# Kernel tuning notes

Measured on AMD Instinct MI355X. Metric: run time of the kernel, lower is better.

Reference implementation:

```python
import jax, jax.numpy as jnp
import numpy as np

N = 100000
E = 800000
D_IN = 64
D_OUT = 64
SCALES = (4, 8)


def setup_inputs() -> dict:
    key = jax.random.key(0)
    ks = jax.random.split(key, 8)
    x = jax.random.normal(ks[0], (N, D_IN), dtype=jnp.float32)
    edge_index = jax.random.randint(ks[1], (2, E), 0, N, dtype=jnp.int64)
    s = 1.0 / np.sqrt(D_IN)
    W1 = jax.random.uniform(ks[2], (D_OUT, D_IN), minval=-s, maxval=s, dtype=jnp.float32)
    b1 = jax.random.uniform(ks[3], (D_OUT,), minval=-s, maxval=s, dtype=jnp.float32)
    W2 = jax.random.uniform(ks[4], (D_OUT, D_IN), minval=-s, maxval=s, dtype=jnp.float32)
    b2 = jax.random.uniform(ks[5], (D_OUT,), minval=-s, maxval=s, dtype=jnp.float32)
    sg = 1.0 / np.sqrt(D_OUT * len(SCALES))
    Wg = jax.random.uniform(ks[6], (D_OUT, D_OUT * len(SCALES)), minval=-sg, maxval=sg, dtype=jnp.float32)
    bg = jax.random.uniform(ks[7], (D_OUT,), minval=-sg, maxval=sg, dtype=jnp.float32)
    return {"x": x, "edge_index": edge_index, "W1": W1, "b1": b1,
            "W2": W2, "b2": b2, "Wg": Wg, "bg": bg}


def _gconv(x, src, tgt, W, b):
    # scatter-add neighbor features: agg[src] += x[tgt]
    agg = jax.ops.segment_sum(x[tgt], src, num_segments=N)  # [N, D_IN]
    counts = jax.ops.segment_sum(jnp.ones((src.shape[0], 1), x.dtype), src,
                                 num_segments=N) + 1e-6     # [N, 1]
    agg = agg / counts
    return agg @ W.T + b                                    # [N, D_OUT]


def reference(x, edge_index, W1, b1, W2, b2, Wg, bg):
    k_max = E // N  # = 8
    outs = []
    for scale, (W, b) in zip(SCALES, ((W1, b1), (W2, b2))):
        scale = min(scale, k_max)
        src = edge_index[0, :N * scale]
        tgt = edge_index[1, :N * scale]
        outs.append(_gconv(x, src, tgt, W, b))
    multi = jnp.concatenate(outs, axis=-1)                   # [N, 2*D_OUT]
    gate = jax.nn.sigmoid(multi @ Wg.T + bg)                 # [N, D_OUT]
    fused = gate * outs[0] + (1.0 - gate) * outs[1]
    return fused
```

## Files before the change

### kernel.cpp

```cpp
#include <hip/hip_runtime.h>
#include <hip/hip_bf16.h>

#define N_NODES 100000
#define E_TOTAL 800000
#define E1      400000
#define D       64
#define CAP     32

#define NPB        256
#define NB         ((N_NODES + NPB - 1) / NPB)
#define BSTRIDE    (NPB * CAP)
#define BCAP       3072
#define EPB        4096
#define NBKT_BLKS  ((E_TOTAL + EPB - 1) / EPB)
#define PREP_TPB   512
#define EPT        (EPB / PREP_TPB)
#define NBP        512

typedef short s16x8 __attribute__((ext_vector_type(8)));
typedef float f32x4 __attribute__((ext_vector_type(4)));
typedef unsigned u32x4 __attribute__((ext_vector_type(4)));

#define WS_CNT     0
#define WS_ENTRIES (N_NODES)
#define WS_W1B     (WS_ENTRIES + N_NODES * CAP)
#define WS_W2B     (WS_W1B + 2048)
#define WS_WGB     (WS_W2B + 2048)
#define WS_BIAS    (WS_WGB + 4096)
#define WS_CUR     (WS_BIAS + 192)
#define WS_XB      (WS_CUR + 512)
#define WS_NEED_BYTES ((size_t)(WS_XB + (size_t)N_NODES * D / 2) * 4)

#define XCONV_BLOCKS ((N_NODES * D / 16 + PREP_TPB - 1) / PREP_TPB)
#define WCONV_BLOCKS 5

__device__ __forceinline__ float ldv(const void* p, size_t idx, int fp32)
{
    return fp32 ? ((const float*)p)[idx]
                : __bfloat162float(((const __hip_bfloat16*)p)[idx]);
}

__device__ __forceinline__ void detect2(const int* ei, const unsigned short* xu,
                                        int* s2, int& e64, int& fp32)
{
    if (threadIdx.x == 0) { s2[0] = 0; s2[1] = 0; }
    __syncthreads();
    if (threadIdx.x < 16 && ei[2 * threadIdx.x + 1] != 0) atomicOr(&s2[0], 1);
    { unsigned u = xu[threadIdx.x]; if (((u >> 7) & 0xFF) >= 0x90) atomicOr(&s2[1], 1); }
    __syncthreads();
    e64 = (s2[0] == 0); fp32 = s2[1];
}

__global__ __launch_bounds__(512) void prep_kernel(
    const void* __restrict__ xv, const int* __restrict__ ei,
    const void* __restrict__ W1v, const void* __restrict__ b1v,
    const void* __restrict__ W2v, const void* __restrict__ b2v,
    const void* __restrict__ Wgv, const void* __restrict__ bgv,
    unsigned* __restrict__ ws, int use_xb)
{
    __shared__ int s2[2];
    __shared__ unsigned hist[NB];
    __shared__ unsigned sc[NBP];
    __shared__ unsigned gbase[NB];
    __shared__ unsigned sorted_s[EPB];
    __shared__ unsigned short bkt_s[EPB];
    int e64, fp32;
    detect2(ei, (const unsigned short*)xv, s2, e64, fp32);

    const int tid = threadIdx.x;

    if (blockIdx.x < NBKT_BLKS) {
        for (int j = tid; j < NB; j += PREP_TPB) hist[j] = 0;
        __syncthreads();

        const int e0 = blockIdx.x * EPB;
        int srcv[EPT], tgtv[EPT];
        if (e64) {
#pragma unroll
            for (int i = 0; i < EPT; ++i) {
                const int e  = e0 + i * PREP_TPB + tid;
                const int ec = min(e, E_TOTAL - 1);
                srcv[i] = (int)((const uint2*)ei)[ec].x;
                tgtv[i] = (int)((const uint2*)ei)[E_TOTAL + ec].x;
                if (e >= E_TOTAL) srcv[i] = -1;
            }
        } else {
#pragma unroll
            for (int i = 0; i < EPT; ++i) {
                const int e  = e0 + i * PREP_TPB + tid;
                const int ec = min(e, E_TOTAL - 1);
                srcv[i] = ei[ec];
                tgtv[i] = ei[E_TOTAL + ec];
                if (e >= E_TOTAL) srcv[i] = -1;
            }
        }

        unsigned recv[EPT], br[EPT];
#pragma unroll
        for (int i = 0; i < EPT; ++i) {
            const int e = e0 + i * PREP_TPB + tid;
            br[i] = 0xFFFFFFFFu;
            if (srcv[i] >= 0) {
                const unsigned b = (unsigned)srcv[i] >> 8;
                const unsigned r = atomicAdd(&hist[b], 1u);
                recv[i] = (unsigned)tgtv[i]
                        | ((e < E1) ? 0x20000u : 0u)
                        | (((unsigned)srcv[i] & (NPB - 1)) << 18);
                br[i] = (b << 16) | r;
            }
        }
        __syncthreads();

        sc[tid] = (tid < NB) ? hist[tid] : 0u;
        __syncthreads();
        for (int s = 1; s < NBP; s <<= 1) {
            const unsigned v = (tid >= s) ? sc[tid - s] : 0u;
            __syncthreads();
            sc[tid] += v;
            __syncthreads();
        }

        for (int j = tid; j < NB; j += PREP_TPB) {
            const unsigned h = hist[j];
            gbase[j] = h ? atomicAdd(ws + WS_CUR + j, h) : 0u;
        }
        __syncthreads();

#pragma unroll
        for (int i = 0; i < EPT; ++i) {
            if (br[i] != 0xFFFFFFFFu) {
                const unsigned b = br[i] >> 16, r = br[i] & 0xFFFFu;
                const unsigned pos = (sc[b] - hist[b]) + r;
                sorted_s[pos] = recv[i];
                bkt_s[pos] = (unsigned short)b;
            }
        }
        __syncthreads();

        const unsigned tot = sc[NB - 1];
        for (unsigned k = tid; k < tot; k += PREP_TPB) {
            const unsigned b = bkt_s[k];
            const unsigned g = gbase[b] + (k - (sc[b] - hist[b]));
            if (g < BCAP)
                ws[WS_ENTRIES + (size_t)b * BSTRIDE + g] = sorted_s[k];
        }
        return;
    }

    const int bx = (int)blockIdx.x - NBKT_BLKS;
    if (bx < XCONV_BLOCKS) {
        if (use_xb && fp32) {
            const int gid = bx * PREP_TPB + tid;
            if (gid < N_NODES * D / 16) {
                __hip_bfloat16* Xb = (__hip_bfloat16*)(ws + WS_XB);
                const f32x4* src4 = (const f32x4*)xv + (size_t)gid * 4;
#pragma unroll
                for (int h = 0; h < 2; ++h) {
                    const f32x4 v0 = src4[2 * h];
                    const f32x4 v1 = src4[2 * h + 1];
                    s16x8 o;
#pragma unroll
                    for (int j = 0; j < 4; ++j) {
                        o[j]     = (short)__bfloat16_as_ushort(__float2bfloat16(v0[j]));
                        o[4 + j] = (short)__bfloat16_as_ushort(__float2bfloat16(v1[j]));
                    }
                    *(s16x8*)(Xb + (size_t)gid * 16 + h * 8) = o;
                }
            }
        }
        return;
    }

    const int gid = (bx - XCONV_BLOCKS) * PREP_TPB + tid;
    __hip_bfloat16* W1b = (__hip_bfloat16*)(ws + WS_W1B);
    __hip_bfloat16* W2b = (__hip_bfloat16*)(ws + WS_W2B);
    __hip_bfloat16* Wgb = (__hip_bfloat16*)(ws + WS_WGB);
    float* bias = (float*)(ws + WS_BIAS);

    if (gid < 2048) {
#pragma unroll
        for (int k = 0; k < 8; ++k) {
            const int i = gid * 8 + k;
            if (i < 4096)       W1b[i]        = __float2bfloat16(ldv(W1v, i, fp32));
            else if (i < 8192)  W2b[i - 4096] = __float2bfloat16(ldv(W2v, i - 4096, fp32));
            else                Wgb[i - 8192] = __float2bfloat16(ldv(Wgv, i - 8192, fp32));
        }
    } else if (gid < 2072) {
        const int j = gid - 2048;
#pragma unroll
        for (int k = 0; k < 8; ++k) {
            const int i = j * 8 + k;
            if (i < 64)       bias[i] = ldv(b1v, i, fp32);
            else if (i < 128) bias[i] = ldv(b2v, i - 64, fp32);
            else              bias[i] = ldv(bgv, i - 128, fp32);
        }
    }
}

__global__ __launch_bounds__(256) void csr_kernel(unsigned* __restrict__ ws)
{
    __shared__ unsigned rec_s[BCAP];
    __shared__ __align__(16) unsigned ent[NPB * CAP];
    __shared__ unsigned n1c[NPB], ctc[NPB], a1[NPB], a2[NPB];

    const int b  = blockIdx.x;
    const int n0 = b * NPB;
    const int nn = min(NPB, N_NODES - n0);

    for (int j = threadIdx.x; j < NPB; j += 256) { n1c[j] = 0; ctc[j] = 0; }
    {
        const u32x4 z = {0u, 0u, 0u, 0u};
        for (int j = threadIdx.x; j < NPB * CAP / 4; j += 256) ((u32x4*)ent)[j] = z;
    }
    const unsigned C = min(ws[WS_CUR + b], (unsigned)BCAP);
    for (unsigned r = threadIdx.x; r < C; r += 256)
        rec_s[r] = ws[WS_ENTRIES + (size_t)b * BSTRIDE + r];
    __syncthreads();

    for (unsigned r = threadIdx.x; r < C; r += 256) {
        const unsigned rec = rec_s[r];
        const unsigned sl  = rec >> 18;
        atomicAdd(&ctc[sl], 1u);
        if (rec & 0x20000u) atomicAdd(&n1c[sl], 1u);
    }
    __syncthreads();
    for (int j = threadIdx.x; j < NPB; j += 256) {
        a1[j] = 0u;
        a2[j] = min(n1c[j], (unsigned)CAP);
    }
    __syncthreads();
    for (unsigned r = threadIdx.x; r < C; r += 256) {
        const unsigned rec = rec_s[r];
        const unsigned sl  = rec >> 18;
        unsigned p;
        if (rec & 0x20000u) p = atomicAdd(&a1[sl], 1u);
        else                p = atomicAdd(&a2[sl], 1u);
        if (p < CAP) ent[sl * CAP + p] = rec & 0x1FFFFu;
    }
    __syncthreads();

    const int tot4 = (nn * CAP) / 4;
    u32x4* dst = (u32x4*)(ws + WS_ENTRIES + (size_t)n0 * CAP);
    const u32x4* srcp = (const u32x4*)ent;
    for (int j = threadIdx.x; j < tot4; j += 256) dst[j] = srcp[j];

    if (threadIdx.x < nn) {
        const unsigned ct = min(ctc[threadIdx.x], 0xFFFFu);
        const unsigned p1 = min(n1c[threadIdx.x], (unsigned)CAP);
        ws[WS_CNT + n0 + threadIdx.x] = ct | (p1 << 16);
    }
}

__global__ __launch_bounds__(256) void fused_kernel(
    const unsigned* __restrict__ ws, const void* __restrict__ xv,
    void* __restrict__ outv, int use_xb)
{
    __shared__ __align__(16) __hip_bfloat16 sS[16][136];
    __shared__ __align__(16) __hip_bfloat16 sO[16][136];
    __shared__ int s2d[2];

    if (threadIdx.x == 0) s2d[0] = 0;
    __syncthreads();
    { unsigned u = ((const unsigned short*)xv)[threadIdx.x];
      if (((u >> 7) & 0xFF) >= 0x90) atomicOr(&s2d[0], 1); }
    __syncthreads();
    const int fp32 = s2d[0];

    const int w    = threadIdx.x >> 6;
    const int lane = threadIdx.x & 63;
    const int base = blockIdx.x * 16;

    unsigned entv[4], cw[4];
#pragma unroll
    for (int i = 0; i < 4; ++i) {
        const int n = base + w * 4 + i;
        cw[i]   = ws[WS_CNT + n];
        entv[i] = ws[WS_ENTRIES + (size_t)n * CAP + (lane & 31)];
    }
    int degc[4], p1c[4]; unsigned degt[4];
#pragma unroll
    for (int i = 0; i < 4; ++i) {
        degt[i] = cw[i] & 0xFFFFu;
        p1c[i]  = (int)(cw[i] >> 16);
        degc[i] = (int)min(degt[i], (unsigned)CAP);
    }

    const int half = lane >> 5;
    const int cc   = lane & 31;

    float s1x[4], s1y[4], s2x[4], s2y[4];
#pragma unroll
    for (int i = 0; i < 4; ++i) { s1x[i] = s1y[i] = s2x[i] = s2y[i] = 0.f; }

    int rmax = 0;
#pragma unroll
    for (int i = 0; i < 4; ++i) rmax = max(rmax, (degc[i] + 1) >> 1);
    rmax = (rmax + 1) & ~1;

    const int direct_f32 = (fp32 && !use_xb);
    if (!direct_f32) {
        const char* xb = fp32 ? (const char*)(ws + WS_XB) : (const char*)xv;
        const unsigned ccb = (unsigned)cc << 2;
#pragma unroll 2
        for (int r = 0; r < rmax; ++r) {
#pragma unroll
            for (int i = 0; i < 4; ++i) {
                const int j = 2 * r + half;
                const unsigned en = (unsigned)__shfl((int)entv[i], j);
                unsigned u = *(const unsigned*)(xb + (size_t)((en << 7) + ccb));
                u = (j < degc[i]) ? u : 0u;
                const float fx = __uint_as_float(u << 16);
                const float fy = __uint_as_float(u & 0xFFFF0000u);
                const float fl = (j < p1c[i]) ? 1.f : 0.f;
                s2x[i] += fx; s2y[i] += fy;
                s1x[i] = fmaf(fl, fx, s1x[i]); s1y[i] = fmaf(fl, fy, s1y[i]);
            }
        }
    } else {
        const char* xb = (const char*)xv;
        const unsigned ccb = (unsigned)cc << 3;
#pragma unroll 2
        for (int r = 0; r < rmax; ++r) {
#pragma unroll
            for (int i = 0; i < 4; ++i) {
                const int j = 2 * r + half;
                const unsigned en = (unsigned)__shfl((int)entv[i], j);
                const uint2 u = *(const uint2*)(xb + (size_t)((en << 8) + ccb));
                const bool val = j < degc[i];
                const float fx = val ? __uint_as_float(u.x) : 0.f;
                const float fy = val ? __uint_as_float(u.y) : 0.f;
                const float fl = (j < p1c[i]) ? 1.f : 0.f;
                s2x[i] += fx; s2y[i] += fy;
                s1x[i] = fmaf(fl, fx, s1x[i]); s1y[i] = fmaf(fl, fy, s1y[i]);
            }
        }
    }

#pragma unroll
    for (int i = 0; i < 4; ++i) {
        const int nl = w * 4 + i;
        float a = s1x[i], b = s1y[i], c = s2x[i], d = s2y[i];
        a += __shfl_xor(a, 32); b += __shfl_xor(b, 32);
        c += __shfl_xor(c, 32); d += __shfl_xor(d, 32);
        const float inv1 = 1.0f / ((float)p1c[i] + 1e-6f);
        const float inv2 = 1.0f / ((float)degt[i] + 1e-6f);
        if (lane < 32) {
            const __hip_bfloat162 p1 = __float22bfloat162_rn({a * inv1, b * inv1});
            const __hip_bfloat162 p2 = __float22bfloat162_rn({c * inv2, d * inv2});
            *(__hip_bfloat162*)&sS[nl][2 * cc]      = p1;
            *(__hip_bfloat162*)&sS[nl][64 + 2 * cc] = p2;
        }
    }
    __syncthreads();

    const int m = lane & 15;
    const int q = lane >> 4;
    const int nd = w * 16 + m;

    const s16x8* W1b = (const s16x8*)(ws + WS_W1B);
    const s16x8* W2b = (const s16x8*)(ws + WS_W2B);
    const s16x8* Wgb = (const s16x8*)(ws + WS_WGB);
    const float* bias = (const float*)(ws + WS_BIAS);

    const s16x8 a1c0 = *(const s16x8*)&sS[m][q * 8];
    const s16x8 a1c1 = *(const s16x8*)&sS[m][32 + q * 8];
    const s16x8 a2c0 = *(const s16x8*)&sS[m][64 + q * 8];
    const s16x8 a2c1 = *(const s16x8*)&sS[m][96 + q * 8];

    f32x4 z = {0.f, 0.f, 0.f, 0.f};
    z = __builtin_amdgcn_mfma_f32_16x16x32_bf16(a1c0, W1b[nd * 8 + q],     z, 0, 0, 0);
    z = __builtin_amdgcn_mfma_f32_16x16x32_bf16(a1c1, W1b[nd * 8 + 4 + q], z, 0, 0, 0);
    f32x4 y = {0.f, 0.f, 0.f, 0.f};
    y = __builtin_amdgcn_mfma_f32_16x16x32_bf16(a2c0, W2b[nd * 8 + q],     y, 0, 0, 0);
    y = __builtin_amdgcn_mfma_f32_16x16x32_bf16(a2c1, W2b[nd * 8 + 4 + q], y, 0, 0, 0);
    const float bb1 = bias[nd], bb2 = bias[64 + nd];
#pragma unroll
    for (int r = 0; r < 4; ++r) { z[r] += bb1; y[r] += bb2; }

#pragma unroll
    for (int r = 0; r < 4; ++r) {
        sO[q * 4 + r][nd]      = __float2bfloat16(z[r]);
        sO[q * 4 + r][64 + nd] = __float2bfloat16(y[r]);
    }
    __syncthreads();

    s16x8 ga[4];
#pragma unroll
    for (int c = 0; c < 4; ++c)
        ga[c] = *(const s16x8*)&sO[m][c * 32 + q * 8];

    f32x4 g4 = {0.f, 0.f, 0.f, 0.f};
#pragma unroll
    for (int c = 0; c < 4; ++c)
        g4 = __builtin_amdgcn_mfma_f32_16x16x32_bf16(ga[c], Wgb[nd * 16 + c * 4 + q], g4, 0, 0, 0);
    const float bbg = bias[128 + nd];

#pragma unroll
    for (int r = 0; r < 4; ++r) {
        const float g = 1.0f / (1.0f + __expf(-(g4[r] + bbg)));
        const float v = g * z[r] + (1.0f - g) * y[r];
        const size_t node = (size_t)(base + q * 4 + r);
        if (fp32) ((float*)outv)[node * 64 + nd] = v;
        else      ((__hip_bfloat16*)outv)[node * 64 + nd] = __float2bfloat16(v);
    }
}

extern "C" void kernel_launch(void* const* d_in, const int* in_sizes, int n_in,
                              void* d_out, int out_size, void* d_ws, size_t ws_size,
                              hipStream_t stream)
{
    const void* x  = d_in[0];
    const int*  ei = (const int*)d_in[1];
    unsigned* ws = (unsigned*)d_ws;

    const int use_xb = (ws_size >= WS_NEED_BYTES) ? 1 : 0;

    hipMemsetAsync(ws + WS_CUR, 0, NB * sizeof(unsigned), stream);
    prep_kernel<<<NBKT_BLKS + XCONV_BLOCKS + WCONV_BLOCKS, PREP_TPB, 0, stream>>>(
        x, ei, d_in[2], d_in[3], d_in[4], d_in[5], d_in[6], d_in[7], ws, use_xb);
    csr_kernel<<<NB, 256, 0, stream>>>(ws);
    fused_kernel<<<N_NODES / 16, 256, 0, stream>>>(ws, x, d_out, use_xb);
}
```

Measured before the change: 151.4 us.

## Merge prep and CSR kernels into one cooperative kernel with grid sync

Folds the bucket-sort prep kernel and the per-bucket CSR build kernel into a single cooperative launch of 512 blocks, separated by a grid-wide barrier, which removes one kernel launch and its drain/fill gap. The sort phase now uses 2048 edges per block and a wave-shuffle scan instead of a barrier-heavy shared-memory scan, and the x bf16 conversion runs as a grid-strided loop over fewer blocks. In exchange it relies on all 512 blocks being co-resident with 48KB of shared memory each. The CSR phase now uses 512 threads, so half the threads idle in per-node loops.

```diff
diff --git a/kernel.cpp b/kernel.cpp
--- a/kernel.cpp
+++ b/kernel.cpp
@@ -1,5 +1,8 @@
 #include <hip/hip_runtime.h>
 #include <hip/hip_bf16.h>
+#include <hip/hip_cooperative_groups.h>
+
+namespace cg = cooperative_groups;
 
 #define N_NODES 100000
 #define E_TOTAL 800000
@@ -11,11 +14,12 @@
 #define NB         ((N_NODES + NPB - 1) / NPB)
 #define BSTRIDE    (NPB * CAP)
 #define BCAP       3072
-#define EPB        4096
-#define NBKT_BLKS  ((E_TOTAL + EPB - 1) / EPB)
-#define PREP_TPB   512
-#define EPT        (EPB / PREP_TPB)
-#define NBP        512
+#define EPB        2048
+#define NSORT      ((E_TOTAL + EPB - 1) / EPB)
+#define K1_TPB     512
+#define EPT        (EPB / K1_TPB)
+#define XCONV_B    120
+#define GRID1      512
 
 typedef short s16x8 __attribute__((ext_vector_type(8)));
 typedef float f32x4 __attribute__((ext_vector_type(4)));
@@ -31,9 +35,6 @@
 #define WS_XB      (WS_CUR + 512)
 #define WS_NEED_BYTES ((size_t)(WS_XB + (size_t)N_NODES * D / 2) * 4)
 
-#define XCONV_BLOCKS ((N_NODES * D / 16 + PREP_TPB - 1) / PREP_TPB)
-#define WCONV_BLOCKS 5
-
 __device__ __forceinline__ float ldv(const void* p, size_t idx, int fp32)
 {
     return fp32 ? ((const float*)p)[idx]
@@ -51,7 +52,7 @@
     e64 = (s2[0] == 0); fp32 = s2[1];
 }
 
-__global__ __launch_bounds__(512) void prep_kernel(
+__global__ __launch_bounds__(512) void build_kernel(
     const void* __restrict__ xv, const int* __restrict__ ei,
     const void* __restrict__ W1v, const void* __restrict__ b1v,
     const void* __restrict__ W2v, const void* __restrict__ b2v,
@@ -59,26 +60,33 @@
     unsigned* __restrict__ ws, int use_xb)
 {
     __shared__ int s2[2];
-    __shared__ unsigned hist[NB];
-    __shared__ unsigned sc[NBP];
-    __shared__ unsigned gbase[NB];
-    __shared__ unsigned sorted_s[EPB];
-    __shared__ unsigned short bkt_s[EPB];
+    __shared__ unsigned wsum[8], wpre[8];
+    __shared__ __align__(16) unsigned lraw[12288];
+
     int e64, fp32;
     detect2(ei, (const unsigned short*)xv, s2, e64, fp32);
 
-    const int tid = threadIdx.x;
-
-    if (blockIdx.x < NBKT_BLKS) {
-        for (int j = tid; j < NB; j += PREP_TPB) hist[j] = 0;
-        __syncthreads();
-
-        const int e0 = blockIdx.x * EPB;
+    const int tid  = threadIdx.x;
+    const int bid  = blockIdx.x;
+    const int lane = tid & 63;
+    const int wid  = tid >> 6;
+
+    if (bid < NSORT) {
+        unsigned* hist   = lraw;
+        unsigned* sc     = lraw + 512;
+        unsigned* gbase  = lraw + 1024;
+        unsigned* sorted = lraw + 1536;
+        unsigned short* bkt = (unsigned short*)(lraw + 1536 + 2048);
+
+        for (int j = tid; j < NB; j += K1_TPB) hist[j] = 0;
+        __syncthreads();
+
+        const int e0 = bid * EPB;
         int srcv[EPT], tgtv[EPT];
         if (e64) {
 #pragma unroll
             for (int i = 0; i < EPT; ++i) {
-                const int e  = e0 + i * PREP_TPB + tid;
+                const int e  = e0 + i * K1_TPB + tid;
                 const int ec = min(e, E_TOTAL - 1);
                 srcv[i] = (int)((const uint2*)ei)[ec].x;
                 tgtv[i] = (int)((const uint2*)ei)[E_TOTAL + ec].x;
@@ -87,7 +95,7 @@
         } else {
 #pragma unroll
             for (int i = 0; i < EPT; ++i) {
-                const int e  = e0 + i * PREP_TPB + tid;
+                const int e  = e0 + i * K1_TPB + tid;
                 const int ec = min(e, E_TOTAL - 1);
                 srcv[i] = ei[ec];
                 tgtv[i] = ei[E_TOTAL + ec];
@@ -98,7 +106,7 @@
         unsigned recv[EPT], br[EPT];
 #pragma unroll
         for (int i = 0; i < EPT; ++i) {
-            const int e = e0 + i * PREP_TPB + tid;
+            const int e = e0 + i * K1_TPB + tid;
             br[i] = 0xFFFFFFFFu;
             if (srcv[i] >= 0) {
                 const unsigned b = (unsigned)srcv[i] >> 8;
@@ -111,16 +119,24 @@
         }
         __syncthreads();
 
-        sc[tid] = (tid < NB) ? hist[tid] : 0u;
-        __syncthreads();
-        for (int s = 1; s < NBP; s <<= 1) {
-            const unsigned v = (tid >= s) ? sc[tid - s] : 0u;
-            __syncthreads();
-            sc[tid] += v;
-            __syncthreads();
-        }
-
-        for (int j = tid; j < NB; j += PREP_TPB) {
+        unsigned v = (tid < NB) ? hist[tid] : 0u;
+#pragma unroll
+        for (int s = 1; s < 64; s <<= 1) {
+            const unsigned t = __shfl_up(v, s);
+            if (lane >= s) v += t;
+        }
+        if (lane == 63) wsum[wid] = v;
+        __syncthreads();
+        if (tid == 0) {
+            unsigned acc = 0;
+#pragma unroll
+            for (int k = 0; k < 8; ++k) { acc += wsum[k]; wpre[k] = acc; }
+        }
+        __syncthreads();
+        if (wid) v += wpre[wid - 1];
+        if (tid < NB) sc[tid] = v;
+
+        for (int j = tid; j < NB; j += K1_TPB) {
             const unsigned h = hist[j];
             gbase[j] = h ? atomicAdd(ws + WS_CUR + j, h) : 0u;
         }
@@ -131,123 +147,118 @@
             if (br[i] != 0xFFFFFFFFu) {
                 const unsigned b = br[i] >> 16, r = br[i] & 0xFFFFu;
                 const unsigned pos = (sc[b] - hist[b]) + r;
-                sorted_s[pos] = recv[i];
-                bkt_s[pos] = (unsigned short)b;
+                sorted[pos] = recv[i];
+                bkt[pos] = (unsigned short)b;
             }
         }
         __syncthreads();
 
         const unsigned tot = sc[NB - 1];
-        for (unsigned k = tid; k < tot; k += PREP_TPB) {
-            const unsigned b = bkt_s[k];
+        for (unsigned k = tid; k < tot; k += K1_TPB) {
+            const unsigned b = bkt[k];
             const unsigned g = gbase[b] + (k - (sc[b] - hist[b]));
             if (g < BCAP)
-                ws[WS_ENTRIES + (size_t)b * BSTRIDE + g] = sorted_s[k];
-        }
-        return;
-    }
-
-    const int bx = (int)blockIdx.x - NBKT_BLKS;
-    if (bx < XCONV_BLOCKS) {
+                ws[WS_ENTRIES + (size_t)b * BSTRIDE + g] = sorted[k];
+        }
+    } else if (bid < NSORT + XCONV_B) {
         if (use_xb && fp32) {
-            const int gid = bx * PREP_TPB + tid;
-            if (gid < N_NODES * D / 16) {
-                __hip_bfloat16* Xb = (__hip_bfloat16*)(ws + WS_XB);
-                const f32x4* src4 = (const f32x4*)xv + (size_t)gid * 4;
-#pragma unroll
-                for (int h = 0; h < 2; ++h) {
-                    const f32x4 v0 = src4[2 * h];
-                    const f32x4 v1 = src4[2 * h + 1];
-                    s16x8 o;
-#pragma unroll
-                    for (int j = 0; j < 4; ++j) {
-                        o[j]     = (short)__bfloat16_as_ushort(__float2bfloat16(v0[j]));
-                        o[4 + j] = (short)__bfloat16_as_ushort(__float2bfloat16(v1[j]));
-                    }
-                    *(s16x8*)(Xb + (size_t)gid * 16 + h * 8) = o;
+            __hip_bfloat16* Xb = (__hip_bfloat16*)(ws + WS_XB);
+            const int cb = bid - NSORT;
+            const int nthr = XCONV_B * K1_TPB;
+            for (int c = cb * K1_TPB + tid; c < N_NODES * D / 8; c += nthr) {
+                const f32x4 v0 = ((const f32x4*)xv)[2 * c];
+                const f32x4 v1 = ((const f32x4*)xv)[2 * c + 1];
+                s16x8 o;
+#pragma unroll
+                for (int j = 0; j < 4; ++j) {
+                    o[j]     = (short)__bfloat16_as_ushort(__float2bfloat16(v0[j]));
+                    o[4 + j] = (short)__bfloat16_as_ushort(__float2bfloat16(v1[j]));
                 }
-            }
-        }
-        return;
-    }
-
-    const int gid = (bx - XCONV_BLOCKS) * PREP_TPB + tid;
-    __hip_bfloat16* W1b = (__hip_bfloat16*)(ws + WS_W1B);
-    __hip_bfloat16* W2b = (__hip_bfloat16*)(ws + WS_W2B);
-    __hip_bfloat16* Wgb = (__hip_bfloat16*)(ws + WS_WGB);
-    float* bias = (float*)(ws + WS_BIAS);
-
-    if (gid < 2048) {
-#pragma unroll
-        for (int k = 0; k < 8; ++k) {
-            const int i = gid * 8 + k;
-            if (i < 4096)       W1b[i]        = __float2bfloat16(ldv(W1v, i, fp32));
-            else if (i < 8192)  W2b[i - 4096] = __float2bfloat16(ldv(W2v, i - 4096, fp32));
-            else                Wgb[i - 8192] = __float2bfloat16(ldv(Wgv, i - 8192, fp32));
-        }
-    } else if (gid < 2072) {
-        const int j = gid - 2048;
-#pragma unroll
-        for (int k = 0; k < 8; ++k) {
-            const int i = j * 8 + k;
-            if (i < 64)       bias[i] = ldv(b1v, i, fp32);
-            else if (i < 128) bias[i] = ldv(b2v, i - 64, fp32);
-            else              bias[i] = ldv(bgv, i - 128, fp32);
-        }
-    }
-}
-
-__global__ __launch_bounds__(256) void csr_kernel(unsigned* __restrict__ ws)
-{
-    __shared__ unsigned rec_s[BCAP];
-    __shared__ __align__(16) unsigned ent[NPB * CAP];
-    __shared__ unsigned n1c[NPB], ctc[NPB], a1[NPB], a2[NPB];
-
-    const int b  = blockIdx.x;
-    const int n0 = b * NPB;
-    const int nn = min(NPB, N_NODES - n0);
-
-    for (int j = threadIdx.x; j < NPB; j += 256) { n1c[j] = 0; ctc[j] = 0; }
-    {
-        const u32x4 z = {0u, 0u, 0u, 0u};
-        for (int j = threadIdx.x; j < NPB * CAP / 4; j += 256) ((u32x4*)ent)[j] = z;
-    }
-    const unsigned C = min(ws[WS_CUR + b], (unsigned)BCAP);
-    for (unsigned r = threadIdx.x; r < C; r += 256)
-        rec_s[r] = ws[WS_ENTRIES + (size_t)b * BSTRIDE + r];
-    __syncthreads();
-
-    for (unsigned r = threadIdx.x; r < C; r += 256) {
-        const unsigned rec = rec_s[r];
-        const unsigned sl  = rec >> 18;
-        atomicAdd(&ctc[sl], 1u);
-        if (rec & 0x20000u) atomicAdd(&n1c[sl], 1u);
-    }
-    __syncthreads();
-    for (int j = threadIdx.x; j < NPB; j += 256) {
-        a1[j] = 0u;
-        a2[j] = min(n1c[j], (unsigned)CAP);
-    }
-    __syncthreads();
-    for (unsigned r = threadIdx.x; r < C; r += 256) {
-        const unsigned rec = rec_s[r];
-        const unsigned sl  = rec >> 18;
-        unsigned p;
-        if (rec & 0x20000u) p = atomicAdd(&a1[sl], 1u);
-        else                p = atomicAdd(&a2[sl], 1u);
-        if (p < CAP) ent[sl * CAP + p] = rec & 0x1FFFFu;
-    }
-    __syncthreads();
-
-    const int tot4 = (nn * CAP) / 4;
-    u32x4* dst = (u32x4*)(ws + WS_ENTRIES + (size_t)n0 * CAP);
-    const u32x4* srcp = (const u32x4*)ent;
-    for (int j = threadIdx.x; j < tot4; j += 256) dst[j] = srcp[j];
-
-    if (threadIdx.x < nn) {
-        const unsigned ct = min(ctc[threadIdx.x], 0xFFFFu);
-        const unsigned p1 = min(n1c[threadIdx.x], (unsigned)CAP);
-        ws[WS_CNT + n0 + threadIdx.x] = ct | (p1 << 16);
+                *(s16x8*)(Xb + (size_t)c * 8) = o;
+            }
+        }
+    } else {
+        __hip_bfloat16* W1b = (__hip_bfloat16*)(ws + WS_W1B);
+        __hip_bfloat16* W2b = (__hip_bfloat16*)(ws + WS_W2B);
+        __hip_bfloat16* Wgb = (__hip_bfloat16*)(ws + WS_WGB);
+        float* bias = (float*)(ws + WS_BIAS);
+        for (int c = tid; c < 2048; c += K1_TPB) {
+#pragma unroll
+            for (int k = 0; k < 8; ++k) {
+                const int i = c * 8 + k;
+                if (i < 4096)       W1b[i]        = __float2bfloat16(ldv(W1v, i, fp32));
+                else if (i < 8192)  W2b[i - 4096] = __float2bfloat16(ldv(W2v, i - 4096, fp32));
+                else                Wgb[i - 8192] = __float2bfloat16(ldv(Wgv, i - 8192, fp32));
+            }
+        }
+        if (tid < 24) {
+#pragma unroll
+            for (int k = 0; k < 8; ++k) {
+                const int i = tid * 8 + k;
+                if (i < 64)       bias[i] = ldv(b1v, i, fp32);
+                else if (i < 128) bias[i] = ldv(b2v, i - 64, fp32);
+                else              bias[i] = ldv(bgv, i - 128, fp32);
+            }
+        }
+    }
+
+    __threadfence();
+    cg::this_grid().sync();
+
+    if (bid < NB) {
+        unsigned* rec_s = lraw;
+        unsigned* ent   = lraw + 3072;
+        unsigned* n1c   = lraw + 11264;
+        unsigned* ctc   = lraw + 11520;
+        unsigned* a1    = lraw + 11776;
+        unsigned* a2    = lraw + 12032;
+
+        const int b  = bid;
+        const int n0 = b * NPB;
+        const int nn = min(NPB, N_NODES - n0);
+
+        for (int j = tid; j < NPB; j += K1_TPB) { n1c[j] = 0; ctc[j] = 0; }
+        {
+            const u32x4 z = {0u, 0u, 0u, 0u};
+            for (int j = tid; j < NPB * CAP / 4; j += K1_TPB) ((u32x4*)ent)[j] = z;
+        }
+        const unsigned C = min(ws[WS_CUR + b], (unsigned)BCAP);
+        for (unsigned r = tid; r < C; r += K1_TPB)
+            rec_s[r] = ws[WS_ENTRIES + (size_t)b * BSTRIDE + r];
+        __syncthreads();
+
+        for (unsigned r = tid; r < C; r += K1_TPB) {
+            const unsigned rec = rec_s[r];
+            const unsigned sl  = rec >> 18;
+            atomicAdd(&ctc[sl], 1u);
+            if (rec & 0x20000u) atomicAdd(&n1c[sl], 1u);
+        }
+        __syncthreads();
+        for (int j = tid; j < NPB; j += K1_TPB) {
+            a1[j] = 0u;
+            a2[j] = min(n1c[j], (unsigned)CAP);
+        }
+        __syncthreads();
+        for (unsigned r = tid; r < C; r += K1_TPB) {
+            const unsigned rec = rec_s[r];
+            const unsigned sl  = rec >> 18;
+            unsigned p;
+            if (rec & 0x20000u) p = atomicAdd(&a1[sl], 1u);
+            else                p = atomicAdd(&a2[sl], 1u);
+            if (p < CAP) ent[sl * CAP + p] = rec & 0x1FFFFu;
+        }
+        __syncthreads();
+
+        const int tot4 = (nn * CAP) / 4;
+        u32x4* dst = (u32x4*)(ws + WS_ENTRIES + (size_t)n0 * CAP);
+        const u32x4* srcp = (const u32x4*)ent;
+        for (int j = tid; j < tot4; j += K1_TPB) dst[j] = srcp[j];
+
+        if (tid < nn) {
+            const unsigned ct = min(ctc[tid], 0xFFFFu);
+            const unsigned p1 = min(n1c[tid], (unsigned)CAP);
+            ws[WS_CNT + n0 + tid] = ct | (p1 << 16);
+        }
     }
 }
 
@@ -413,11 +424,20 @@
     const int*  ei = (const int*)d_in[1];
     unsigned* ws = (unsigned*)d_ws;
 
-    const int use_xb = (ws_size >= WS_NEED_BYTES) ? 1 : 0;
+    int use_xb = (ws_size >= WS_NEED_BYTES) ? 1 : 0;
 
     hipMemsetAsync(ws + WS_CUR, 0, NB * sizeof(unsigned), stream);
-    prep_kernel<<<NBKT_BLKS + XCONV_BLOCKS + WCONV_BLOCKS, PREP_TPB, 0, stream>>>(
-        x, ei, d_in[2], d_in[3], d_in[4], d_in[5], d_in[6], d_in[7], ws, use_xb);
-    csr_kernel<<<NB, 256, 0, stream>>>(ws);
+
+    const void* W1v = d_in[2]; const void* b1v = d_in[3];
+    const void* W2v = d_in[4]; const void* b2v = d_in[5];
+    const void* Wgv = d_in[6]; const void* bgv = d_in[7];
+    void* args[] = {
+        (void*)&x, (void*)&ei,
+        (void*)&W1v, (void*)&b1v, (void*)&W2v, (void*)&b2v,
+        (void*)&Wgv, (void*)&bgv, (void*)&ws, (void*)&use_xb
+    };
+    hipLaunchCooperativeKernel((void*)build_kernel, dim3(GRID1), dim3(K1_TPB),
+                               args, 0, stream);
+
     fused_kernel<<<N_NODES / 16, 256, 0, stream>>>(ws, x, d_out, use_xb);
 }
```

Result: slower. 351.6 us (+132.3%).

## Fuse CSR build into fused kernel, use wave-shuffle scan, halve edges per sort block

Applied to the files above, without the earlier changes.

Removes the separate csr_kernel. Each fused workgroup now reloads its whole 256-node bucket of records into shared memory and builds per-node neighbor lists for only its 16 nodes, and a remap of block IDs places the 16 workgroups of one bucket on the same XCD for L2 reuse. The prefix scan in prep moves from a block-wide shared-memory loop to per-wave shuffles plus a small cross-wave step, and edges per sort block go from 4096 to 2048 for more parallelism. The tradeoff is that each bucket's records are read 16 times instead of once and every fused block does extra scanning work, in exchange for one fewer launch and no global CSR write and read.

```diff
diff --git a/kernel.cpp b/kernel.cpp
--- a/kernel.cpp
+++ b/kernel.cpp
@@ -11,11 +11,14 @@
 #define NB         ((N_NODES + NPB - 1) / NPB)
 #define BSTRIDE    (NPB * CAP)
 #define BCAP       3072
-#define EPB        4096
-#define NBKT_BLKS  ((E_TOTAL + EPB - 1) / EPB)
+#define EPB        2048
+#define NSORT      ((E_TOTAL + EPB - 1) / EPB)
 #define PREP_TPB   512
 #define EPT        (EPB / PREP_TPB)
-#define NBP        512
+
+#define FUSED_NWG  (N_NODES / 16)
+#define NWG_Q      (FUSED_NWG / 8)
+#define NWG_R      (FUSED_NWG % 8)
 
 typedef short s16x8 __attribute__((ext_vector_type(8)));
 typedef float f32x4 __attribute__((ext_vector_type(4)));
@@ -59,21 +62,26 @@
     unsigned* __restrict__ ws, int use_xb)
 {
     __shared__ int s2[2];
-    __shared__ unsigned hist[NB];
-    __shared__ unsigned sc[NBP];
-    __shared__ unsigned gbase[NB];
+    __shared__ unsigned wsum[8], wpre[8];
+    __shared__ unsigned hist[512];
+    __shared__ unsigned sc[512];
+    __shared__ unsigned gbase[512];
     __shared__ unsigned sorted_s[EPB];
     __shared__ unsigned short bkt_s[EPB];
+
     int e64, fp32;
     detect2(ei, (const unsigned short*)xv, s2, e64, fp32);
 
-    const int tid = threadIdx.x;
-
-    if (blockIdx.x < NBKT_BLKS) {
-        for (int j = tid; j < NB; j += PREP_TPB) hist[j] = 0;
-        __syncthreads();
-
-        const int e0 = blockIdx.x * EPB;
+    const int tid  = threadIdx.x;
+    const int bid  = blockIdx.x;
+    const int lane = tid & 63;
+    const int wid  = tid >> 6;
+
+    if (bid < NSORT) {
+        hist[tid] = 0;
+        __syncthreads();
+
+        const int e0 = bid * EPB;
         int srcv[EPT], tgtv[EPT];
         if (e64) {
 #pragma unroll
@@ -111,14 +119,22 @@
         }
         __syncthreads();
 
-        sc[tid] = (tid < NB) ? hist[tid] : 0u;
-        __syncthreads();
-        for (int s = 1; s < NBP; s <<= 1) {
-            const unsigned v = (tid >= s) ? sc[tid - s] : 0u;
-            __syncthreads();
-            sc[tid] += v;
-            __syncthreads();
-        }
+        unsigned v = hist[tid];
+#pragma unroll
+        for (int s = 1; s < 64; s <<= 1) {
+            const unsigned t = __shfl_up(v, s);
+            if (lane >= s) v += t;
+        }
+        if (lane == 63) wsum[wid] = v;
+        __syncthreads();
+        if (tid == 0) {
+            unsigned acc = 0;
+#pragma unroll
+            for (int k = 0; k < 8; ++k) { acc += wsum[k]; wpre[k] = acc; }
+        }
+        __syncthreads();
+        if (wid) v += wpre[wid - 1];
+        sc[tid] = v;
 
         for (int j = tid; j < NB; j += PREP_TPB) {
             const unsigned h = hist[j];
@@ -147,7 +163,7 @@
         return;
     }
 
-    const int bx = (int)blockIdx.x - NBKT_BLKS;
+    const int bx = bid - NSORT;
     if (bx < XCONV_BLOCKS) {
         if (use_xb && fp32) {
             const int gid = bx * PREP_TPB + tid;
@@ -197,92 +213,77 @@
     }
 }
 
-__global__ __launch_bounds__(256) void csr_kernel(unsigned* __restrict__ ws)
-{
-    __shared__ unsigned rec_s[BCAP];
-    __shared__ __align__(16) unsigned ent[NPB * CAP];
-    __shared__ unsigned n1c[NPB], ctc[NPB], a1[NPB], a2[NPB];
-
-    const int b  = blockIdx.x;
-    const int n0 = b * NPB;
-    const int nn = min(NPB, N_NODES - n0);
-
-    for (int j = threadIdx.x; j < NPB; j += 256) { n1c[j] = 0; ctc[j] = 0; }
-    {
-        const u32x4 z = {0u, 0u, 0u, 0u};
-        for (int j = threadIdx.x; j < NPB * CAP / 4; j += 256) ((u32x4*)ent)[j] = z;
-    }
-    const unsigned C = min(ws[WS_CUR + b], (unsigned)BCAP);
-    for (unsigned r = threadIdx.x; r < C; r += 256)
-        rec_s[r] = ws[WS_ENTRIES + (size_t)b * BSTRIDE + r];
-    __syncthreads();
-
-    for (unsigned r = threadIdx.x; r < C; r += 256) {
-        const unsigned rec = rec_s[r];
-        const unsigned sl  = rec >> 18;
-        atomicAdd(&ctc[sl], 1u);
-        if (rec & 0x20000u) atomicAdd(&n1c[sl], 1u);
-    }
-    __syncthreads();
-    for (int j = threadIdx.x; j < NPB; j += 256) {
-        a1[j] = 0u;
-        a2[j] = min(n1c[j], (unsigned)CAP);
-    }
-    __syncthreads();
-    for (unsigned r = threadIdx.x; r < C; r += 256) {
-        const unsigned rec = rec_s[r];
-        const unsigned sl  = rec >> 18;
-        unsigned p;
-        if (rec & 0x20000u) p = atomicAdd(&a1[sl], 1u);
-        else                p = atomicAdd(&a2[sl], 1u);
-        if (p < CAP) ent[sl * CAP + p] = rec & 0x1FFFFu;
-    }
-    __syncthreads();
-
-    const int tot4 = (nn * CAP) / 4;
-    u32x4* dst = (u32x4*)(ws + WS_ENTRIES + (size_t)n0 * CAP);
-    const u32x4* srcp = (const u32x4*)ent;
-    for (int j = threadIdx.x; j < tot4; j += 256) dst[j] = srcp[j];
-
-    if (threadIdx.x < nn) {
-        const unsigned ct = min(ctc[threadIdx.x], 0xFFFFu);
-        const unsigned p1 = min(n1c[threadIdx.x], (unsigned)CAP);
-        ws[WS_CNT + n0 + threadIdx.x] = ct | (p1 << 16);
-    }
-}
-
 __global__ __launch_bounds__(256) void fused_kernel(
     const unsigned* __restrict__ ws, const void* __restrict__ xv,
     void* __restrict__ outv, int use_xb)
 {
+    __shared__ __align__(16) unsigned rec_s[BCAP];
+    __shared__ unsigned ent_l[16 * CAP];
+    __shared__ unsigned ctc[16], n1c[16], a1s[16], a2s[16];
     __shared__ __align__(16) __hip_bfloat16 sS[16][136];
     __shared__ __align__(16) __hip_bfloat16 sO[16][136];
-    __shared__ int s2d[2];
-
-    if (threadIdx.x == 0) s2d[0] = 0;
-    __syncthreads();
-    { unsigned u = ((const unsigned short*)xv)[threadIdx.x];
+    __shared__ int s2d[1];
+
+    const int tid = threadIdx.x;
+
+    if (tid == 0) s2d[0] = 0;
+    __syncthreads();
+    { unsigned u = ((const unsigned short*)xv)[tid];
       if (((u >> 7) & 0xFF) >= 0x90) atomicOr(&s2d[0], 1); }
+
+    const int p  = (int)blockIdx.x;
+    const int xx = p & 7, ii = p >> 3;
+    const int bidl = (xx < NWG_R) ? xx * (NWG_Q + 1) + ii
+                                  : NWG_R * (NWG_Q + 1) + (xx - NWG_R) * NWG_Q + ii;
+
+    const int b    = bidl >> 4;
+    const int w0   = (bidl & 15) << 4;
+    const int base = bidl * 16;
+
+    const unsigned C = min(ws[WS_CUR + b], (unsigned)BCAP);
+    for (unsigned r = tid; r < C; r += 256)
+        rec_s[r] = ws[WS_ENTRIES + (size_t)b * BSTRIDE + r];
+    if (tid < 16) { ctc[tid] = 0; n1c[tid] = 0; }
+    {
+        ent_l[tid] = 0; ent_l[256 + tid] = 0;
+    }
     __syncthreads();
     const int fp32 = s2d[0];
 
-    const int w    = threadIdx.x >> 6;
-    const int lane = threadIdx.x & 63;
-    const int base = blockIdx.x * 16;
-
-    unsigned entv[4], cw[4];
+    for (unsigned r = tid; r < C; r += 256) {
+        const unsigned rec = rec_s[r];
+        const unsigned k = (rec >> 18) - (unsigned)w0;
+        if (k < 16u) {
+            atomicAdd(&ctc[k], 1u);
+            if (rec & 0x20000u) atomicAdd(&n1c[k], 1u);
+        }
+    }
+    __syncthreads();
+    if (tid < 16) { a1s[tid] = 0u; a2s[tid] = min(n1c[tid], (unsigned)CAP); }
+    __syncthreads();
+    for (unsigned r = tid; r < C; r += 256) {
+        const unsigned rec = rec_s[r];
+        const unsigned k = (rec >> 18) - (unsigned)w0;
+        if (k < 16u) {
+            unsigned pos;
+            if (rec & 0x20000u) pos = atomicAdd(&a1s[k], 1u);
+            else                pos = atomicAdd(&a2s[k], 1u);
+            if (pos < CAP) ent_l[k * CAP + pos] = rec & 0x1FFFFu;
+        }
+    }
+    __syncthreads();
+
+    const int w    = tid >> 6;
+    const int lane = tid & 63;
+
+    unsigned entv[4], degt[4]; int degc[4], p1c[4];
 #pragma unroll
     for (int i = 0; i < 4; ++i) {
-        const int n = base + w * 4 + i;
-        cw[i]   = ws[WS_CNT + n];
-        entv[i] = ws[WS_ENTRIES + (size_t)n * CAP + (lane & 31)];
-    }
-    int degc[4], p1c[4]; unsigned degt[4];
-#pragma unroll
-    for (int i = 0; i < 4; ++i) {
-        degt[i] = cw[i] & 0xFFFFu;
-        p1c[i]  = (int)(cw[i] >> 16);
+        const int k = w * 4 + i;
+        degt[i] = ctc[k];
+        p1c[i]  = (int)min(n1c[k], (unsigned)CAP);
         degc[i] = (int)min(degt[i], (unsigned)CAP);
+        entv[i] = ent_l[k * CAP + (lane & 31)];
     }
 
     const int half = lane >> 5;
@@ -339,13 +340,13 @@
 #pragma unroll
     for (int i = 0; i < 4; ++i) {
         const int nl = w * 4 + i;
-        float a = s1x[i], b = s1y[i], c = s2x[i], d = s2y[i];
-        a += __shfl_xor(a, 32); b += __shfl_xor(b, 32);
+        float a = s1x[i], bq = s1y[i], c = s2x[i], d = s2y[i];
+        a += __shfl_xor(a, 32); bq += __shfl_xor(bq, 32);
         c += __shfl_xor(c, 32); d += __shfl_xor(d, 32);
         const float inv1 = 1.0f / ((float)p1c[i] + 1e-6f);
         const float inv2 = 1.0f / ((float)degt[i] + 1e-6f);
         if (lane < 32) {
-            const __hip_bfloat162 p1 = __float22bfloat162_rn({a * inv1, b * inv1});
+            const __hip_bfloat162 p1 = __float22bfloat162_rn({a * inv1, bq * inv1});
             const __hip_bfloat162 p2 = __float22bfloat162_rn({c * inv2, d * inv2});
             *(__hip_bfloat162*)&sS[nl][2 * cc]      = p1;
             *(__hip_bfloat162*)&sS[nl][64 + 2 * cc] = p2;
@@ -415,9 +416,8 @@
 
     const int use_xb = (ws_size >= WS_NEED_BYTES) ? 1 : 0;
 
-    hipMemsetAsync(ws + WS_CUR, 0, NB * sizeof(unsigned), stream);
-    prep_kernel<<<NBKT_BLKS + XCONV_BLOCKS + WCONV_BLOCKS, PREP_TPB, 0, stream>>>(
+    hipMemsetAsync(ws + WS_CUR, 0, 512 * sizeof(unsigned), stream);
+    prep_kernel<<<NSORT + XCONV_BLOCKS + WCONV_BLOCKS, PREP_TPB, 0, stream>>>(
         x, ei, d_in[2], d_in[3], d_in[4], d_in[5], d_in[6], d_in[7], ws, use_xb);
-    csr_kernel<<<NB, 256, 0, stream>>>(ws);
-    fused_kernel<<<N_NODES / 16, 256, 0, stream>>>(ws, x, d_out, use_xb);
+    fused_kernel<<<FUSED_NWG, 256, 0, stream>>>(ws, x, d_out, use_xb);
 }
```

New measurement: 166.4 us. 10.0% more time.

## Replace global-atomic bucket scatter with fixed per-block cell slots

Applied to the files above, without the earlier changes.

The edge bucketing pass stops using a block-wide prefix scan and global atomic cursors. Each prep block now writes a fixed slot of PER=40 records per destination bucket into a strided span, marking valid records with a high bit. This removes the scan, the global atomics and the memset launch. The CSR kernel then reads the whole fixed span and filters on the valid bit. The cost is reading and writing many empty cells (196*40 per block), and edges beyond 40 per bucket per block are silently dropped. That is a correctness risk that depends on the random input distribution, which averages about 21 per cell.

```diff
diff --git a/kernel.cpp b/kernel.cpp
--- a/kernel.cpp
+++ b/kernel.cpp
@@ -10,12 +10,12 @@
 #define NPB        256
 #define NB         ((N_NODES + NPB - 1) / NPB)
 #define BSTRIDE    (NPB * CAP)
-#define BCAP       3072
 #define EPB        4096
 #define NBKT_BLKS  ((E_TOTAL + EPB - 1) / EPB)
+#define PER        40
+#define SPAN       (NBKT_BLKS * PER)
 #define PREP_TPB   512
 #define EPT        (EPB / PREP_TPB)
-#define NBP        512
 
 typedef short s16x8 __attribute__((ext_vector_type(8)));
 typedef float f32x4 __attribute__((ext_vector_type(4)));
@@ -27,8 +27,8 @@
 #define WS_W2B     (WS_W1B + 2048)
 #define WS_WGB     (WS_W2B + 2048)
 #define WS_BIAS    (WS_WGB + 4096)
-#define WS_CUR     (WS_BIAS + 192)
-#define WS_XB      (WS_CUR + 512)
+#define WS_REC390  (WS_BIAS + 192)
+#define WS_XB      (WS_REC390 + SPAN)
 #define WS_NEED_BYTES ((size_t)(WS_XB + (size_t)N_NODES * D / 2) * 4)
 
 #define XCONV_BLOCKS ((N_NODES * D / 16 + PREP_TPB - 1) / PREP_TPB)
@@ -59,18 +59,20 @@
     unsigned* __restrict__ ws, int use_xb)
 {
     __shared__ int s2[2];
-    __shared__ unsigned hist[NB];
-    __shared__ unsigned sc[NBP];
-    __shared__ unsigned gbase[NB];
-    __shared__ unsigned sorted_s[EPB];
-    __shared__ unsigned short bkt_s[EPB];
+    __shared__ unsigned hist[512];
+    __shared__ __align__(16) unsigned cells[NB * PER];
+
     int e64, fp32;
     detect2(ei, (const unsigned short*)xv, s2, e64, fp32);
 
     const int tid = threadIdx.x;
 
     if (blockIdx.x < NBKT_BLKS) {
-        for (int j = tid; j < NB; j += PREP_TPB) hist[j] = 0;
+        hist[tid] = 0;
+        {
+            const u32x4 z = {0u, 0u, 0u, 0u};
+            for (int j = tid; j < NB * PER / 4; j += PREP_TPB) ((u32x4*)cells)[j] = z;
+        }
         __syncthreads();
 
         const int e0 = blockIdx.x * EPB;
@@ -95,54 +97,28 @@
             }
         }
 
-        unsigned recv[EPT], br[EPT];
 #pragma unroll
         for (int i = 0; i < EPT; ++i) {
             const int e = e0 + i * PREP_TPB + tid;
-            br[i] = 0xFFFFFFFFu;
             if (srcv[i] >= 0) {
                 const unsigned b = (unsigned)srcv[i] >> 8;
                 const unsigned r = atomicAdd(&hist[b], 1u);
-                recv[i] = (unsigned)tgtv[i]
-                        | ((e < E1) ? 0x20000u : 0u)
-                        | (((unsigned)srcv[i] & (NPB - 1)) << 18);
-                br[i] = (b << 16) | r;
+                if (r < PER)
+                    cells[b * PER + r] = (unsigned)tgtv[i]
+                                       | ((e < E1) ? 0x20000u : 0u)
+                                       | (((unsigned)srcv[i] & 0xFFu) << 18)
+                                       | 0x80000000u;
             }
         }
         __syncthreads();
 
-        sc[tid] = (tid < NB) ? hist[tid] : 0u;
-        __syncthreads();
-        for (int s = 1; s < NBP; s <<= 1) {
-            const unsigned v = (tid >= s) ? sc[tid - s] : 0u;
-            __syncthreads();
-            sc[tid] += v;
-            __syncthreads();
-        }
-
-        for (int j = tid; j < NB; j += PREP_TPB) {
-            const unsigned h = hist[j];
-            gbase[j] = h ? atomicAdd(ws + WS_CUR + j, h) : 0u;
-        }
-        __syncthreads();
-
-#pragma unroll
-        for (int i = 0; i < EPT; ++i) {
-            if (br[i] != 0xFFFFFFFFu) {
-                const unsigned b = br[i] >> 16, r = br[i] & 0xFFFFu;
-                const unsigned pos = (sc[b] - hist[b]) + r;
-                sorted_s[pos] = recv[i];
-                bkt_s[pos] = (unsigned short)b;
-            }
-        }
-        __syncthreads();
-
-        const unsigned tot = sc[NB - 1];
-        for (unsigned k = tid; k < tot; k += PREP_TPB) {
-            const unsigned b = bkt_s[k];
-            const unsigned g = gbase[b] + (k - (sc[b] - hist[b]));
-            if (g < BCAP)
-                ws[WS_ENTRIES + (size_t)b * BSTRIDE + g] = sorted_s[k];
+        unsigned* dstbase = ws + WS_ENTRIES + (size_t)blockIdx.x * PER;
+        unsigned* rec390  = ws + WS_REC390 + (size_t)blockIdx.x * PER;
+        for (int j = tid; j < NB * PER; j += PREP_TPB) {
+            const int b = j / PER;
+            const int r = j - b * PER;
+            if (b == NB - 1) rec390[r] = cells[j];
+            else             dstbase[(size_t)b * BSTRIDE + r] = cells[j];
         }
         return;
     }
@@ -199,43 +175,48 @@
 
 __global__ __launch_bounds__(256) void csr_kernel(unsigned* __restrict__ ws)
 {
-    __shared__ unsigned rec_s[BCAP];
+    __shared__ __align__(16) unsigned rec_s[SPAN];
     __shared__ __align__(16) unsigned ent[NPB * CAP];
     __shared__ unsigned n1c[NPB], ctc[NPB], a1[NPB], a2[NPB];
 
     const int b  = blockIdx.x;
     const int n0 = b * NPB;
     const int nn = min(NPB, N_NODES - n0);
-
-    for (int j = threadIdx.x; j < NPB; j += 256) { n1c[j] = 0; ctc[j] = 0; }
+    const unsigned* span = (b == NB - 1) ? (ws + WS_REC390)
+                                         : (ws + WS_ENTRIES + (size_t)b * BSTRIDE);
+
+    if (threadIdx.x < NPB) { n1c[threadIdx.x] = 0; ctc[threadIdx.x] = 0; }
     {
         const u32x4 z = {0u, 0u, 0u, 0u};
         for (int j = threadIdx.x; j < NPB * CAP / 4; j += 256) ((u32x4*)ent)[j] = z;
-    }
-    const unsigned C = min(ws[WS_CUR + b], (unsigned)BCAP);
-    for (unsigned r = threadIdx.x; r < C; r += 256)
-        rec_s[r] = ws[WS_ENTRIES + (size_t)b * BSTRIDE + r];
-    __syncthreads();
-
-    for (unsigned r = threadIdx.x; r < C; r += 256) {
+        for (int j = threadIdx.x; j < SPAN / 4; j += 256)
+            ((u32x4*)rec_s)[j] = ((const u32x4*)span)[j];
+    }
+    __syncthreads();
+
+    for (int r = threadIdx.x; r < SPAN; r += 256) {
         const unsigned rec = rec_s[r];
-        const unsigned sl  = rec >> 18;
-        atomicAdd(&ctc[sl], 1u);
-        if (rec & 0x20000u) atomicAdd(&n1c[sl], 1u);
-    }
-    __syncthreads();
-    for (int j = threadIdx.x; j < NPB; j += 256) {
-        a1[j] = 0u;
-        a2[j] = min(n1c[j], (unsigned)CAP);
-    }
-    __syncthreads();
-    for (unsigned r = threadIdx.x; r < C; r += 256) {
+        if (rec & 0x80000000u) {
+            const unsigned sl = (rec >> 18) & 0xFFu;
+            atomicAdd(&ctc[sl], 1u);
+            if (rec & 0x20000u) atomicAdd(&n1c[sl], 1u);
+        }
+    }
+    __syncthreads();
+    if (threadIdx.x < NPB) {
+        a1[threadIdx.x] = 0u;
+        a2[threadIdx.x] = min(n1c[threadIdx.x], (unsigned)CAP);
+    }
+    __syncthreads();
+    for (int r = threadIdx.x; r < SPAN; r += 256) {
         const unsigned rec = rec_s[r];
-        const unsigned sl  = rec >> 18;
-        unsigned p;
-        if (rec & 0x20000u) p = atomicAdd(&a1[sl], 1u);
-        else                p = atomicAdd(&a2[sl], 1u);
-        if (p < CAP) ent[sl * CAP + p] = rec & 0x1FFFFu;
+        if (rec & 0x80000000u) {
+            const unsigned sl = (rec >> 18) & 0xFFu;
+            unsigned p;
+            if (rec & 0x20000u) p = atomicAdd(&a1[sl], 1u);
+            else                p = atomicAdd(&a2[sl], 1u);
+            if (p < CAP) ent[sl * CAP + p] = rec & 0x1FFFFu;
+        }
     }
     __syncthreads();
 
@@ -257,7 +238,7 @@
 {
     __shared__ __align__(16) __hip_bfloat16 sS[16][136];
     __shared__ __align__(16) __hip_bfloat16 sO[16][136];
-    __shared__ int s2d[2];
+    __shared__ int s2d[1];
 
     if (threadIdx.x == 0) s2d[0] = 0;
     __syncthreads();
@@ -415,7 +396,6 @@
 
     const int use_xb = (ws_size >= WS_NEED_BYTES) ? 1 : 0;
 
-    hipMemsetAsync(ws + WS_CUR, 0, NB * sizeof(unsigned), stream);
     prep_kernel<<<NBKT_BLKS + XCONV_BLOCKS + WCONV_BLOCKS, PREP_TPB, 0, stream>>>(
         x, ei, d_in[2], d_in[3], d_in[4], d_in[5], d_in[6], d_in[7], ws, use_xb);
     csr_kernel<<<NB, 256, 0, stream>>>(ws);
```

Result: no change. 153.3 us (+1.3%).
